# Optimization experiments

Hardware: AMD Instinct MI355X
Metric: run time of the kernel (lower is better)

The kernel has to match this reference:

```python
import jax, jax.numpy as jnp
import numpy as np

B, L_IN, C_IN, C_SKIP, C_OUT, DEPTH = 8, 512, 512, 512, 512, 4
D_INNER, D_STATE, D_CONV, DT_RANK = 1024, 16, 4, 32
EPS = 1e-5


def rmsnorm(x, w):
    return x * jax.lax.rsqrt(jnp.mean(x * x, axis=-1, keepdims=True) + EPS) * w


def layernorm(x, w, b):
    m = jnp.mean(x, axis=-1, keepdims=True)
    v = jnp.mean((x - m) ** 2, axis=-1, keepdims=True)
    return (x - m) * jax.lax.rsqrt(v + EPS) * w + b


def selective_scan(u, dt, A, Bm, Cm, Dp):
    # u, dt: (B, L, Di); A: (Di, N); Bm, Cm: (B, L, N); Dp: (Di,)
    def step(h, inp):
        dt_t, B_t, C_t, u_t = inp  # (B,Di),(B,N),(B,N),(B,Di)
        dA = jnp.exp(dt_t[..., None] * A)            # (B,Di,N)
        h = dA * h + (dt_t * u_t)[..., None] * B_t[:, None, :]
        y = jnp.einsum('bdn,bn->bd', h, C_t)
        return h, y

    Bb, L, Di = u.shape
    h0 = jnp.zeros((Bb, Di, A.shape[1]), u.dtype)
    xs = (dt.transpose(1, 0, 2), Bm.transpose(1, 0, 2),
          Cm.transpose(1, 0, 2), u.transpose(1, 0, 2))
    _, ys = jax.lax.scan(step, h0, xs)               # ys: (L,B,Di)
    return ys.transpose(1, 0, 2) + u * Dp


def mamba_block(x, in_w, cw, cb, xp_w, dtw, dtb, A_log, Dp, ow, ob):
    xz = x @ in_w.T                                   # (B,L,2*Di)
    xc, z = jnp.split(xz, 2, axis=-1)
    # causal depthwise conv, kernel D_CONV
    xc_t = jax.lax.conv_general_dilated(
        xc.transpose(0, 2, 1), cw[:, None, :], (1,), [(D_CONV - 1, 0)],
        feature_group_count=D_INNER,
        dimension_numbers=('NCH', 'OIH', 'NCH'))
    xc = jax.nn.silu((xc_t + cb[None, :, None]).transpose(0, 2, 1))
    xdbc = xc @ xp_w.T                                # (B,L,DT_RANK+2N)
    dtp = xdbc[..., :DT_RANK]
    Bm = xdbc[..., DT_RANK:DT_RANK + D_STATE]
    Cm = xdbc[..., DT_RANK + D_STATE:]
    dt = jax.nn.softplus(dtp @ dtw.T + dtb)
    A = -jnp.exp(A_log)
    y = selective_scan(xc, dt, A, Bm, Cm, Dp)
    return (y * jax.nn.silu(z)) @ ow.T + ob


def forward(motion_input, skip_feats, embed, w_up, b_up, w1, b1, rms_w, w2, b2,
            ln_w, ln_b, in_proj_w, conv_w, conv_b, x_proj_w, dt_proj_w,
            dt_proj_b, A_log, D_param, out_proj_w, out_proj_b,
            norm_f_w, norm_f_b):
    Bb, Lin, C = motion_input.shape
    # ConvTranspose1d(C, C, kernel=2, stride=2): non-overlapping expansion
    up = jnp.einsum('blc,cok->blko', motion_input, w_up)
    up = up.reshape(Bb, Lin * 2, C) + b_up            # (B, 2L, C)
    x = jnp.concatenate([up, skip_feats], axis=-1)    # (B, 2L, C+skip)
    # MLP: Linear -> RMSNorm -> SiLU -> Linear
    x = jax.nn.silu(rmsnorm(x @ w1.T + b1, rms_w)) @ w2.T + b2
    # MotionMamba: add embed, depth residual mamba blocks, final norm
    x = x + embed[:, None, :]
    for i in range(DEPTH):
        x = x + mamba_block(layernorm(x, ln_w[i], ln_b[i]), in_proj_w[i],
                            conv_w[i], conv_b[i], x_proj_w[i], dt_proj_w[i],
                            dt_proj_b[i], A_log[i], D_param[i],
                            out_proj_w[i], out_proj_b[i])
    return layernorm(x, norm_f_w, norm_f_b)


def setup_inputs():
    key = jax.random.key(0)
    ks = jax.random.split(key, 16)
    f = lambda k, sh: jax.random.normal(k, sh, jnp.float32) * 0.02
    inp = {}
    inp['motion_input'] = jax.random.normal(ks[0], (B, L_IN, C_IN), jnp.float32)
    inp['skip_feats'] = jax.random.normal(ks[1], (B, 2 * L_IN, C_SKIP), jnp.float32)
    inp['embed'] = jax.random.normal(ks[2], (B, C_OUT), jnp.float32)
    inp['w_up'] = f(ks[3], (C_IN, C_IN, 2))
    inp['b_up'] = jnp.zeros((C_IN,), jnp.float32)
    inp['w1'] = f(ks[4], (C_OUT, C_IN + C_SKIP))
    inp['b1'] = jnp.zeros((C_OUT,), jnp.float32)
    inp['rms_w'] = jnp.ones((C_OUT,), jnp.float32)
    inp['w2'] = f(ks[5], (C_OUT, C_OUT))
    inp['b2'] = jnp.zeros((C_OUT,), jnp.float32)
    inp['ln_w'] = jnp.ones((DEPTH, C_OUT), jnp.float32)
    inp['ln_b'] = jnp.zeros((DEPTH, C_OUT), jnp.float32)
    inp['in_proj_w'] = f(ks[6], (DEPTH, 2 * D_INNER, C_OUT))
    inp['conv_w'] = f(ks[7], (DEPTH, D_INNER, D_CONV))
    inp['conv_b'] = jnp.zeros((DEPTH, D_INNER), jnp.float32)
    inp['x_proj_w'] = f(ks[8], (DEPTH, DT_RANK + 2 * D_STATE, D_INNER))
    inp['dt_proj_w'] = f(ks[9], (DEPTH, D_INNER, DT_RANK))
    inp['dt_proj_b'] = jnp.full((DEPTH, D_INNER), -4.0, jnp.float32)
    inp['A_log'] = jnp.log(jnp.tile(jnp.arange(1, D_STATE + 1, dtype=jnp.float32), (DEPTH, D_INNER, 1)))
    inp['D_param'] = jnp.ones((DEPTH, D_INNER), jnp.float32)
    inp['out_proj_w'] = f(ks[10], (DEPTH, C_OUT, D_INNER))
    inp['out_proj_b'] = jnp.zeros((DEPTH, C_OUT), jnp.float32)
    inp['norm_f_w'] = jnp.ones((C_OUT,), jnp.float32)
    inp['norm_f_b'] = jnp.zeros((C_OUT,), jnp.float32)
    return inp


def reference(motion_input, skip_feats, embed, w_up, b_up, w1, b1, rms_w, w2,
              b2, ln_w, ln_b, in_proj_w, conv_w, conv_b, x_proj_w, dt_proj_w,
              dt_proj_b, A_log, D_param, out_proj_w, out_proj_b,
              norm_f_w, norm_f_b):
    return forward(motion_input, skip_feats, embed, w_up, b_up, w1, b1, rms_w,
                   w2, b2, ln_w, ln_b, in_proj_w, conv_w, conv_b, x_proj_w,
                   dt_proj_w, dt_proj_b, A_log, D_param, out_proj_w,
                   out_proj_b, norm_f_w, norm_f_b)
```

## Files before the change

kernel.cpp:

```cpp
#include <hip/hip_runtime.h>
#include <cstdint>
#include <cstddef>

#define DEV_INLINE __device__ __forceinline__

static constexpr float EPS = 1e-5f;

DEV_INLINE float sigmoidf_(float x) { return 1.0f / (1.0f + __expf(-x)); }
DEV_INLINE float siluf_(float x) { return x * sigmoidf_(x); }
DEV_INLINE float softplus_fast(float x) {
    return fmaxf(x, 0.0f) + __logf(1.0f + __expf(-fabsf(x)));
}
DEV_INLINE unsigned short f2bf(float x) {
    unsigned u = __builtin_bit_cast(unsigned, x);
    u += 0x7FFFu + ((u >> 16) & 1u);
    return (unsigned short)(u >> 16);
}
DEV_INLINE float bf2f(unsigned short s) {
    unsigned u = ((unsigned)s) << 16;
    return __builtin_bit_cast(float, u);
}

typedef __attribute__((ext_vector_type(8))) short bf16x8;
typedef __attribute__((ext_vector_type(4))) float f32x4;

DEV_INLINE void gload16(const unsigned short* src, char* ldsdst) {
    __builtin_amdgcn_global_load_lds(
        (const __attribute__((address_space(1))) unsigned int*)src,
        (__attribute__((address_space(3))) unsigned int*)ldsdst, 16, 0, 0);
}

DEV_INLINE void cvt8(const float* __restrict__ s, unsigned short* __restrict__ d, int t) {
    float4 f0 = *(const float4*)(s + (size_t)t * 8);
    float4 f1 = *(const float4*)(s + (size_t)t * 8 + 4);
    union { unsigned short u[8]; uint4 v; } pk;
    pk.u[0] = f2bf(f0.x); pk.u[1] = f2bf(f0.y); pk.u[2] = f2bf(f0.z); pk.u[3] = f2bf(f0.w);
    pk.u[4] = f2bf(f1.x); pk.u[5] = f2bf(f1.y); pk.u[6] = f2bf(f1.z); pk.u[7] = f2bf(f1.w);
    *(uint4*)(d + (size_t)t * 8) = pk.v;
}

__global__ __launch_bounds__(256) void prep_all(
    const float* __restrict__ motion, const float* __restrict__ wup,
    const float* __restrict__ w1, const float* __restrict__ w2,
    const float* __restrict__ in_proj_w, const float* __restrict__ out_proj_w,
    const float* __restrict__ x_proj_w, const float* __restrict__ dt_proj_w,
    unsigned short* __restrict__ mbf, unsigned short* __restrict__ wupT,
    unsigned short* __restrict__ w1b, unsigned short* __restrict__ w2b,
    unsigned short* __restrict__ lw)
{
    int bid = (int)blockIdx.x, tid = (int)threadIdx.x;
    if (bid < 1024) {
        cvt8(motion, mbf, bid * 256 + tid);
    } else if (bid < 2048) {
        int t = (bid - 1024) * 256 + tid;
        int c = t >> 9, o = t & 511;
        float2 v = *(const float2*)(wup + (size_t)t * 2);
        wupT[(size_t)o * 512 + c] = f2bf(v.x);
        wupT[262144 + (size_t)o * 512 + c] = f2bf(v.y);
    } else if (bid < 2304) {
        cvt8(w1, w1b, (bid - 2048) * 256 + tid);
    } else if (bid < 2432) {
        cvt8(w2, w2b, (bid - 2304) * 256 + tid);
    } else {
        int r = bid - 2432;
        int layer = r / 816;
        int lb = r - layer * 816;
        unsigned short* base = lw + (size_t)layer * 1671168;
        if (lb < 512) {
            cvt8(in_proj_w + (size_t)layer * 1048576, base, lb * 256 + tid);
        } else if (lb < 768) {
            cvt8(out_proj_w + (size_t)layer * 524288, base + 1048576,
                 (lb - 512) * 256 + tid);
        } else if (lb < 800) {
            cvt8(x_proj_w + (size_t)layer * 65536, base + 1572864,
                 (lb - 768) * 256 + tid);
        } else {
            cvt8(dt_proj_w + (size_t)layer * 32768, base + 1638400,
                 (lb - 800) * 256 + tid);
        }
    }
}

template <int ACT, bool ACC, bool EMBED, bool OBF>
__global__ __launch_bounds__(256) void gemm_mfma(
    const unsigned short* __restrict__ A, int lda,
    const unsigned short* __restrict__ W, int ldw,
    void* __restrict__ Cv, int ldc, int N, int K, int gx,
    const float* __restrict__ bias, const float* __restrict__ embed)
{
    __shared__ unsigned short Asm[2][128 * 64];
    __shared__ unsigned short Wsm[2][128 * 64];
    const int tid = (int)threadIdx.x;
    const int lane = tid & 63;
    const int wv = tid >> 6;
    const int wm = wv >> 1, wn = wv & 1;

    const int nwg = (int)gridDim.x;
    const int lin = (int)blockIdx.x;
    const int logical = (lin & 7) * (nwg >> 3) + (lin >> 3);
    const int by = logical / gx;
    const int bx = logical - by * gx;
    const int bm = by * 128, bn = bx * 128;

    f32x4 acc[4][4] = {};
    const int l8 = lane >> 3;
    const int wc = lane & 7;
    const int wcg = wc ^ l8;
    const int NT = K >> 6;

    {
        char* aB = (char*)Asm[0];
        char* bB = (char*)Wsm[0];
#pragma unroll
        for (int i = 0; i < 4; ++i) {
            int rb = (i * 4 + wv) * 8;
            gload16(W + (size_t)(bn + rb + l8) * ldw + wcg * 8, bB + rb * 128);
            gload16(A + (size_t)(bm + rb + l8) * lda + wcg * 8, aB + rb * 128);
        }
    }
    __syncthreads();

    for (int t = 0; t < NT; ++t) {
        const int cur = t & 1;
        if (t + 1 < NT) {
            const int k1 = (t + 1) << 6;
            char* aB = (char*)Asm[cur ^ 1];
            char* bB = (char*)Wsm[cur ^ 1];
#pragma unroll
            for (int i = 0; i < 4; ++i) {
                int rb = (i * 4 + wv) * 8;
                gload16(W + (size_t)(bn + rb + l8) * ldw + k1 + wcg * 8, bB + rb * 128);
                gload16(A + (size_t)(bm + rb + l8) * lda + k1 + wcg * 8, aB + rb * 128);
            }
        }
        const char* aB = (const char*)Asm[cur];
        const char* bB = (const char*)Wsm[cur];
        const int rA = wm * 64 + (lane & 15);
        const int rB = wn * 64 + (lane & 15);
        const int q = lane >> 4;
#pragma unroll
        for (int kk = 0; kk < 2; ++kk) {
            bf16x8 af[4], bfr[4];
#pragma unroll
            for (int mi = 0; mi < 4; ++mi) {
                int row = rA + mi * 16;
                int ch = (kk * 4 + q) ^ (row & 7);
                af[mi] = *(const bf16x8*)(aB + row * 128 + ch * 16);
            }
#pragma unroll
            for (int ni = 0; ni < 4; ++ni) {
                int row = rB + ni * 16;
                int ch = (kk * 4 + q) ^ (row & 7);
                bfr[ni] = *(const bf16x8*)(bB + row * 128 + ch * 16);
            }
#pragma unroll
            for (int mi = 0; mi < 4; ++mi)
#pragma unroll
                for (int ni = 0; ni < 4; ++ni)
                    acc[mi][ni] = __builtin_amdgcn_mfma_f32_16x16x32_bf16(
                        af[mi], bfr[ni], acc[mi][ni], 0, 0, 0);
        }
        __syncthreads();
    }

    const int cn = lane & 15;
    const int r0 = (lane >> 4) * 4;
    const int eb = EMBED ? (bm >> 10) * N : 0;
#pragma unroll
    for (int ni = 0; ni < 4; ++ni) {
        int col = bn + wn * 64 + ni * 16 + cn;
        float add = bias ? bias[col] : 0.0f;
        if (EMBED) add += embed[eb + col];
#pragma unroll
        for (int mi = 0; mi < 4; ++mi) {
#pragma unroll
            for (int r = 0; r < 4; ++r) {
                int row = bm + wm * 64 + mi * 16 + r0 + r;
                float v = acc[mi][ni][r] + add;
                if (ACT == 1) v = softplus_fast(v);
                if (OBF) {
                    ((unsigned short*)Cv)[(size_t)row * ldc + col] = f2bf(v);
                } else {
                    float* p = (float*)Cv + (size_t)row * ldc + col;
                    if (ACC) *p += v; else *p = v;
                }
            }
        }
    }
}

template <int ACT, bool ACC, bool EMBED, bool OBF, bool UPS>
__global__ __launch_bounds__(256) void gemm_mfma64(
    const unsigned short* __restrict__ A, int lda,
    const unsigned short* __restrict__ W, int ldw,
    void* __restrict__ Cv, int ldc, int N, int K, int gx,
    const float* __restrict__ bias, const float* __restrict__ embed)
{
    __shared__ unsigned short Asm[2][64 * 64];
    __shared__ unsigned short Wsm[2][64 * 64];
    const int tid = (int)threadIdx.x;
    const int lane = tid & 63;
    const int wv = tid >> 6;
    const int wm = wv >> 1, wn = wv & 1;

    const int nwg = (int)gridDim.x;
    const int lin = (int)blockIdx.x;
    const int logical = (lin & 7) * (nwg >> 3) + (lin >> 3);
    const int by = logical / gx;
    const int bx = logical - by * gx;
    const int bm = by * 64, bn = bx * 64;

    f32x4 acc[2][2] = {};
    const int l8 = lane >> 3;
    const int wc = lane & 7;
    const int wcg = wc ^ l8;
    const int NT = K >> 6;

    {
        char* aB = (char*)Asm[0];
        char* bB = (char*)Wsm[0];
#pragma unroll
        for (int i = 0; i < 2; ++i) {
            int rb = (i * 4 + wv) * 8;
            gload16(W + (size_t)(bn + rb + l8) * ldw + wcg * 8, bB + rb * 128);
            gload16(A + (size_t)(bm + rb + l8) * lda + wcg * 8, aB + rb * 128);
        }
    }
    __syncthreads();

    for (int t = 0; t < NT; ++t) {
        const int cur = t & 1;
        if (t + 1 < NT) {
            const int k1 = (t + 1) << 6;
            char* aB = (char*)Asm[cur ^ 1];
            char* bB = (char*)Wsm[cur ^ 1];
#pragma unroll
            for (int i = 0; i < 2; ++i) {
                int rb = (i * 4 + wv) * 8;
                gload16(W + (size_t)(bn + rb + l8) * ldw + k1 + wcg * 8, bB + rb * 128);
                gload16(A + (size_t)(bm + rb + l8) * lda + k1 + wcg * 8, aB + rb * 128);
            }
        }
        const char* aB = (const char*)Asm[cur];
        const char* bB = (const char*)Wsm[cur];
        const int rA = wm * 32 + (lane & 15);
        const int rB = wn * 32 + (lane & 15);
        const int q = lane >> 4;
#pragma unroll
        for (int kk = 0; kk < 2; ++kk) {
            bf16x8 af[2], bfr[2];
#pragma unroll
            for (int mi = 0; mi < 2; ++mi) {
                int row = rA + mi * 16;
                int ch = (kk * 4 + q) ^ (row & 7);
                af[mi] = *(const bf16x8*)(aB + row * 128 + ch * 16);
            }
#pragma unroll
            for (int ni = 0; ni < 2; ++ni) {
                int row = rB + ni * 16;
                int ch = (kk * 4 + q) ^ (row & 7);
                bfr[ni] = *(const bf16x8*)(bB + row * 128 + ch * 16);
            }
#pragma unroll
            for (int mi = 0; mi < 2; ++mi)
#pragma unroll
                for (int ni = 0; ni < 2; ++ni)
                    acc[mi][ni] = __builtin_amdgcn_mfma_f32_16x16x32_bf16(
                        af[mi], bfr[ni], acc[mi][ni], 0, 0, 0);
        }
        __syncthreads();
    }

    const int cn = lane & 15;
    const int r0 = (lane >> 4) * 4;
    const int eb = EMBED ? (bm >> 10) * N : 0;
#pragma unroll
    for (int ni = 0; ni < 2; ++ni) {
        int col = bn + wn * 32 + ni * 16 + cn;
        float add = bias ? bias[UPS ? (col & 511) : col] : 0.0f;
        if (EMBED) add += embed[eb + col];
#pragma unroll
        for (int mi = 0; mi < 2; ++mi) {
#pragma unroll
            for (int r = 0; r < 4; ++r) {
                int row = bm + wm * 32 + mi * 16 + r0 + r;
                float v = acc[mi][ni][r] + add;
                if (ACT == 1) v = softplus_fast(v);
                if (UPS) {
                    size_t ad = (size_t)row * 2048 + ((col >> 9) << 10) + (col & 511);
                    ((unsigned short*)Cv)[ad] = f2bf(v);
                } else if (OBF) {
                    ((unsigned short*)Cv)[(size_t)row * ldc + col] = f2bf(v);
                } else {
                    float* p = (float*)Cv + (size_t)row * ldc + col;
                    if (ACC) *p += v; else *p = v;
                }
            }
        }
    }
}

__global__ __launch_bounds__(256) void gemm_dt(
    const unsigned short* __restrict__ xdbc,
    const unsigned short* __restrict__ wdt,
    const float* __restrict__ bias,
    unsigned short* __restrict__ out)
{
    __shared__ unsigned short S[128 * 136];
    const int tid = (int)threadIdx.x;
    const int lane = tid & 63;
    const int wv = tid >> 6;
    const int wm = wv >> 1, wn = wv & 1;

    const int lin = (int)blockIdx.x;
    const int logical = (lin & 7) * 64 + (lin >> 3);
    const int bm = (logical >> 3) * 128;
    const int bn = (logical & 7) * 128;

    const int fr = lane & 15;
    const int q = lane >> 4;

    bf16x8 af[4], wf[4];
#pragma unroll
    for (int mi = 0; mi < 4; ++mi)
        af[mi] = *(const bf16x8*)(xdbc + (size_t)(bm + wm * 64 + mi * 16 + fr) * 64 + q * 8);
#pragma unroll
    for (int ni = 0; ni < 4; ++ni)
        wf[ni] = *(const bf16x8*)(wdt + (size_t)(bn + wn * 64 + ni * 16 + fr) * 32 + q * 8);

    f32x4 acc[4][4] = {};
#pragma unroll
    for (int mi = 0; mi < 4; ++mi)
#pragma unroll
        for (int ni = 0; ni < 4; ++ni)
            acc[mi][ni] = __builtin_amdgcn_mfma_f32_16x16x32_bf16(
                af[mi], wf[ni], acc[mi][ni], 0, 0, 0);

    const int cn = lane & 15;
    const int r0 = (lane >> 4) * 4;
#pragma unroll
    for (int ni = 0; ni < 4; ++ni) {
        int lcol = wn * 64 + ni * 16 + cn;
        float add = bias[bn + lcol];
#pragma unroll
        for (int mi = 0; mi < 4; ++mi) {
#pragma unroll
            for (int r = 0; r < 4; ++r) {
                int lrow = wm * 64 + mi * 16 + r0 + r;
                S[lrow * 136 + lcol] = f2bf(softplus_fast(acc[mi][ni][r] + add));
            }
        }
    }
    __syncthreads();

    const int row = tid >> 1;
    const int half = tid & 1;
    const unsigned short* src = S + row * 136 + half * 64;
    unsigned short* dst = out + (size_t)(bm + row) * 1024 + bn + half * 64;
#pragma unroll
    for (int k = 0; k < 8; ++k) {
        uint4 v = *(const uint4*)(src + k * 8);
        *(uint4*)(dst + k * 8) = v;
    }
}

__global__ __launch_bounds__(128) void gemm_xdbc(
    const unsigned short* __restrict__ A,
    const unsigned short* __restrict__ W,
    unsigned short* __restrict__ C)
{
    __shared__ unsigned short Asm[64 * 64];
    __shared__ unsigned short Wsm[64 * 64];
    const int tid = (int)threadIdx.x;
    const int lane = tid & 63;
    const int w = tid >> 6;
    const int bm = blockIdx.x * 64;
    const int l8 = lane >> 3, wc = lane & 7, wcg = wc ^ l8;
    char* aB = (char*)Asm;
    char* bB = (char*)Wsm;

    f32x4 acc[2][4] = {};

    for (int k0 = 0; k0 < 1024; k0 += 64) {
#pragma unroll
        for (int i = 0; i < 4; ++i) {
            int rb = (i * 2 + w) * 8;
            gload16(A + (size_t)(bm + rb + l8) * 1024 + k0 + wcg * 8, aB + rb * 128);
            gload16(W + (size_t)(rb + l8) * 1024 + k0 + wcg * 8, bB + rb * 128);
        }
        __syncthreads();
        const int rA = w * 32 + (lane & 15);
        const int rB = (lane & 15);
        const int q = lane >> 4;
#pragma unroll
        for (int kk = 0; kk < 2; ++kk) {
            bf16x8 af[2], bfr[4];
#pragma unroll
            for (int mi = 0; mi < 2; ++mi) {
                int row = rA + mi * 16;
                int ch = (kk * 4 + q) ^ (row & 7);
                af[mi] = *(const bf16x8*)(aB + row * 128 + ch * 16);
            }
#pragma unroll
            for (int ni = 0; ni < 4; ++ni) {
                int row = rB + ni * 16;
                int ch = (kk * 4 + q) ^ (row & 7);
                bfr[ni] = *(const bf16x8*)(bB + row * 128 + ch * 16);
            }
#pragma unroll
            for (int mi = 0; mi < 2; ++mi)
#pragma unroll
                for (int ni = 0; ni < 4; ++ni)
                    acc[mi][ni] = __builtin_amdgcn_mfma_f32_16x16x32_bf16(
                        af[mi], bfr[ni], acc[mi][ni], 0, 0, 0);
        }
        __syncthreads();
    }
    const int cn = lane & 15;
    const int r0 = (lane >> 4) * 4;
#pragma unroll
    for (int mi = 0; mi < 2; ++mi)
#pragma unroll
        for (int ni = 0; ni < 4; ++ni)
#pragma unroll
            for (int r = 0; r < 4; ++r) {
                int row = bm + w * 32 + mi * 16 + r0 + r;
                C[(size_t)row * 64 + ni * 16 + cn] = f2bf(acc[mi][ni][r]);
            }
}

__global__ __launch_bounds__(256) void concat_skip(
    const float* __restrict__ skip, unsigned short* __restrict__ x0)
{
    int t = blockIdx.x * 256 + (int)threadIdx.x;
    int row = t >> 6;
    int c8 = (t & 63) << 3;
    const float* s = skip + (size_t)row * 512 + c8;
    float4 f0 = *(const float4*)s;
    float4 f1 = *(const float4*)(s + 4);
    union { unsigned short u[8]; uint4 v; } pk;
    pk.u[0] = f2bf(f0.x); pk.u[1] = f2bf(f0.y); pk.u[2] = f2bf(f0.z); pk.u[3] = f2bf(f0.w);
    pk.u[4] = f2bf(f1.x); pk.u[5] = f2bf(f1.y); pk.u[6] = f2bf(f1.z); pk.u[7] = f2bf(f1.w);
    *(uint4*)(x0 + (size_t)row * 1024 + 512 + c8) = pk.v;
}

template <bool BFOUT>
__global__ __launch_bounds__(256) void layernorm_k(
    const float* __restrict__ x, void* __restrict__ outp,
    const float* __restrict__ w, const float* __restrict__ b)
{
    const int row = blockIdx.x * 4 + ((int)threadIdx.x >> 6);
    const int lane = (int)threadIdx.x & 63;
    const float* xr = x + (size_t)row * 512;
    float4 v0 = *(const float4*)(xr + lane * 4);
    float4 v1 = *(const float4*)(xr + 256 + lane * 4);
    float s = v0.x + v0.y + v0.z + v0.w + v1.x + v1.y + v1.z + v1.w;
    float q = v0.x*v0.x + v0.y*v0.y + v0.z*v0.z + v0.w*v0.w
            + v1.x*v1.x + v1.y*v1.y + v1.z*v1.z + v1.w*v1.w;
#pragma unroll
    for (int o = 32; o; o >>= 1) {
        s += __shfl_xor(s, o, 64);
        q += __shfl_xor(q, o, 64);
    }
    const float mean = s * (1.0f / 512.0f);
    const float var = q * (1.0f / 512.0f) - mean * mean;
    const float rstd = rsqrtf(var + EPS);
    float4 w0 = *(const float4*)(w + lane * 4);
    float4 w1 = *(const float4*)(w + 256 + lane * 4);
    float4 b0 = *(const float4*)(b + lane * 4);
    float4 b1 = *(const float4*)(b + 256 + lane * 4);
    float4 o0, o1;
    o0.x = (v0.x - mean) * rstd * w0.x + b0.x;
    o0.y = (v0.y - mean) * rstd * w0.y + b0.y;
    o0.z = (v0.z - mean) * rstd * w0.z + b0.z;
    o0.w = (v0.w - mean) * rstd * w0.w + b0.w;
    o1.x = (v1.x - mean) * rstd * w1.x + b1.x;
    o1.y = (v1.y - mean) * rstd * w1.y + b1.y;
    o1.z = (v1.z - mean) * rstd * w1.z + b1.z;
    o1.w = (v1.w - mean) * rstd * w1.w + b1.w;
    if (BFOUT) {
        unsigned short* ob = (unsigned short*)outp + (size_t)row * 512;
        union { unsigned short u[4]; uint2 v; } p0, p1;
        p0.u[0] = f2bf(o0.x); p0.u[1] = f2bf(o0.y); p0.u[2] = f2bf(o0.z); p0.u[3] = f2bf(o0.w);
        p1.u[0] = f2bf(o1.x); p1.u[1] = f2bf(o1.y); p1.u[2] = f2bf(o1.z); p1.u[3] = f2bf(o1.w);
        *(uint2*)(ob + lane * 4) = p0.v;
        *(uint2*)(ob + 256 + lane * 4) = p1.v;
    } else {
        float* orow = (float*)outp + (size_t)row * 512;
        *(float4*)(orow + lane * 4) = o0;
        *(float4*)(orow + 256 + lane * 4) = o1;
    }
}

__global__ __launch_bounds__(256) void rms_silu_k(
    const float* __restrict__ x, unsigned short* __restrict__ o,
    const float* __restrict__ w)
{
    const int row = blockIdx.x * 4 + ((int)threadIdx.x >> 6);
    const int lane = (int)threadIdx.x & 63;
    const float* xr = x + (size_t)row * 512;
    float4 v0 = *(const float4*)(xr + lane * 4);
    float4 v1 = *(const float4*)(xr + 256 + lane * 4);
    float q = v0.x*v0.x + v0.y*v0.y + v0.z*v0.z + v0.w*v0.w
            + v1.x*v1.x + v1.y*v1.y + v1.z*v1.z + v1.w*v1.w;
#pragma unroll
    for (int of = 32; of; of >>= 1) q += __shfl_xor(q, of, 64);
    const float scale = rsqrtf(q * (1.0f / 512.0f) + EPS);
    float4 w0 = *(const float4*)(w + lane * 4);
    float4 w1 = *(const float4*)(w + 256 + lane * 4);
    union { unsigned short u[4]; uint2 v; } p0, p1;
    p0.u[0] = f2bf(siluf_(v0.x * scale * w0.x));
    p0.u[1] = f2bf(siluf_(v0.y * scale * w0.y));
    p0.u[2] = f2bf(siluf_(v0.z * scale * w0.z));
    p0.u[3] = f2bf(siluf_(v0.w * scale * w0.w));
    p1.u[0] = f2bf(siluf_(v1.x * scale * w1.x));
    p1.u[1] = f2bf(siluf_(v1.y * scale * w1.y));
    p1.u[2] = f2bf(siluf_(v1.z * scale * w1.z));
    p1.u[3] = f2bf(siluf_(v1.w * scale * w1.w));
    unsigned short* ob = o + (size_t)row * 512;
    *(uint2*)(ob + lane * 4) = p0.v;
    *(uint2*)(ob + 256 + lane * 4) = p1.v;
}

__global__ __launch_bounds__(256) void conv_silu_k2(
    const unsigned short* __restrict__ xz, unsigned short* __restrict__ ub,
    const float* __restrict__ cw, const float* __restrict__ cb)
{
    int t = blockIdx.x * 256 + (int)threadIdx.x;
    int d = t & 1023;
    int bc = t >> 10;
    int b = bc >> 4, ch = bc & 15;
    int l0 = ch * 64;
    float4 w4 = *(const float4*)(cw + (size_t)d * 4);
    float bias = cb[d];
    const unsigned short* src = xz + ((size_t)(b * 1024 + l0)) * 2048 + d;
    unsigned short* dst = ub + ((size_t)(b * 1024 + l0)) * 1024 + d;
    float x0 = 0.f, x1 = 0.f, x2 = 0.f;
    if (l0 > 0) {
        x0 = bf2f(src[-(size_t)3 * 2048]);
        x1 = bf2f(src[-(size_t)2 * 2048]);
        x2 = bf2f(src[-(size_t)1 * 2048]);
    }
    for (int l = 0; l < 64; ++l) {
        float x3 = bf2f(src[(size_t)l * 2048]);
        float v = fmaf(x0, w4.x, fmaf(x1, w4.y, fmaf(x2, w4.z, fmaf(x3, w4.w, bias))));
        dst[(size_t)l * 1024] = f2bf(siluf_(v));
        x0 = x1; x1 = x2; x2 = x3;
    }
}

template <int CTRL>
DEV_INLINE float dpp_f(float x) {
    int yi = __builtin_amdgcn_update_dpp(
        0, __builtin_bit_cast(int, x), CTRL, 0xF, 0xF, true);
    return __builtin_bit_cast(float, yi);
}

template <int PHASE>
__global__ __launch_bounds__(256) void scan5(
    const unsigned short* __restrict__ dtp,
    const unsigned short* ubf,
    unsigned short* ybf,
    const unsigned short* __restrict__ xdbc,
    const unsigned short* __restrict__ zbf,
    float* __restrict__ hp,
    const float* __restrict__ A_log,
    const float* __restrict__ Dp)
{
    __shared__ float SDT2[16][260];
    __shared__ float SB[32][20];
    __shared__ float SC[PHASE == 2 ? 32 : 1][20];
    __shared__ float YS[PHASE == 2 ? 32 : 1][68];

    const int lin = (int)blockIdx.x;
    const int logical = (lin & 7) * 256 + (lin >> 3);
    const int gg = logical & 15;
    const int t2 = logical >> 4;
    const int ch = t2 & 15, b = t2 >> 4;
    if (PHASE == 1 && ch == 15) return;
    const int tid = (int)threadIdx.x;
    const int dl = tid >> 2, q = tid & 2 ? (tid & 3) : (tid & 3);
    const int qq = tid & 3;
    const int dblk = gg << 6;
    const int d = dblk + dl;
    const int m0 = b * 1024 + ch * 64;

    float An[4];
#pragma unroll
    for (int j = 0; j < 4; ++j)
        An[j] = -__expf(A_log[(size_t)d * 16 + qq * 4 + j]);

    float h[4] = {};
    float prod[4] = {1.f, 1.f, 1.f, 1.f};
    if (PHASE == 2) {
        const float* hpb = hp + (((size_t)(b * 1024 + d)) * 16) * 32 + qq * 8;
        for (int cc = 0; cc < ch; ++cc) {
            float4 v0 = *(const float4*)(hpb + cc * 32);
            float4 v1 = *(const float4*)(hpb + cc * 32 + 4);
            h[0] = fmaf(v0.y, h[0], v0.x);
            h[1] = fmaf(v0.w, h[1], v0.z);
            h[2] = fmaf(v1.y, h[2], v1.x);
            h[3] = fmaf(v1.w, h[3], v1.z);
        }
    }

    const int sl2 = tid >> 4;
    const int sdg = (tid & 15) * 4;
    const int bcr = (tid & 127) >> 2;
    const int bne = (tid & 3) << 2;

    for (int s = 0; s < 2; ++s) {
        const int lbase = s * 32;
        {
            size_t r0 = (size_t)(m0 + lbase + 2 * sl2);
            uint2 dA = *(const uint2*)(dtp + r0 * 1024 + dblk + sdg);
            uint2 dB = *(const uint2*)(dtp + (r0 + 1) * 1024 + dblk + sdg);
            uint2 uA = *(const uint2*)(ubf + r0 * 1024 + dblk + sdg);
            uint2 uB = *(const uint2*)(ubf + (r0 + 1) * 1024 + dblk + sdg);
            const unsigned short* da = (const unsigned short*)&dA;
            const unsigned short* db = (const unsigned short*)&dB;
            const unsigned short* ua = (const unsigned short*)&uA;
            const unsigned short* ub2 = (const unsigned short*)&uB;
#pragma unroll
            for (int j = 0; j < 4; ++j) {
                float d0 = bf2f(da[j]), d1 = bf2f(db[j]);
                float4 wv = {d0, d0 * bf2f(ua[j]), d1, d1 * bf2f(ub2[j])};
                *(float4*)&SDT2[sl2][(sdg + j) * 4] = wv;
            }
        }
        {
            size_t gr = (size_t)(m0 + lbase + bcr);
            if (tid < 128) {
                uint2 Bu = *(const uint2*)(xdbc + gr * 64 + 32 + bne);
                const unsigned short* bb = (const unsigned short*)&Bu;
                float4 bv = {bf2f(bb[0]), bf2f(bb[1]), bf2f(bb[2]), bf2f(bb[3])};
                *(float4*)&SB[bcr][bne] = bv;
            } else if (PHASE == 2) {
                uint2 Cu = *(const uint2*)(xdbc + gr * 64 + 48 + bne);
                const unsigned short* cc2 = (const unsigned short*)&Cu;
                float4 cv = {bf2f(cc2[0]), bf2f(cc2[1]), bf2f(cc2[2]), bf2f(cc2[3])};
                *(float4*)&SC[bcr][bne] = cv;
            }
        }
        __syncthreads();

        for (int l2 = 0; l2 < 16; ++l2) {
            float4 sd = *(const float4*)&SDT2[l2][dl * 4];
            float4 B0 = *(const float4*)&SB[2 * l2][qq * 4];
            float4 B1 = *(const float4*)&SB[2 * l2 + 1][qq * 4];
            float p0 = 0.0f, p1 = 0.0f;
            float4 C0, C1;
            if (PHASE == 2) {
                C0 = *(const float4*)&SC[2 * l2][qq * 4];
                C1 = *(const float4*)&SC[2 * l2 + 1][qq * 4];
            }
            const float* B0p = (const float*)&B0;
            const float* B1p = (const float*)&B1;
            const float* C0p = (const float*)&C0;
            const float* C1p = (const float*)&C1;
#pragma unroll
            for (int j = 0; j < 4; ++j) {
                float e0 = __expf(sd.x * An[j]);
                if (PHASE == 1) prod[j] *= e0;
                h[j] = fmaf(e0, h[j], sd.y * B0p[j]);
                if (PHASE == 2) p0 = fmaf(h[j], C0p[j], p0);
                float e1 = __expf(sd.z * An[j]);
                if (PHASE == 1) prod[j] *= e1;
                h[j] = fmaf(e1, h[j], sd.w * B1p[j]);
                if (PHASE == 2) p1 = fmaf(h[j], C1p[j], p1);
            }
            if (PHASE == 2) {
                p0 += dpp_f<0xB1>(p0);
                p0 += dpp_f<0x4E>(p0);
                p1 += dpp_f<0xB1>(p1);
                p1 += dpp_f<0x4E>(p1);
                if (qq == 0) {
                    YS[2 * l2][dl] = p0;
                    YS[2 * l2 + 1][dl] = p1;
                }
            }
        }
        __syncthreads();

        if (PHASE == 2) {
            const int row = tid >> 3;
            const int e8 = (tid & 7) * 8;
            size_t gr = (size_t)(m0 + lbase + row);
            float4 p40 = *(const float4*)&YS[row][e8];
            float4 p41 = *(const float4*)&YS[row][e8 + 4];
            uint4 uu = *(const uint4*)(ubf + gr * 1024 + dblk + e8);
            uint4 zz = *(const uint4*)(zbf + gr * 2048 + 1024 + dblk + e8);
            float4 D0 = *(const float4*)(Dp + dblk + e8);
            float4 D1 = *(const float4*)(Dp + dblk + e8 + 4);
            const unsigned short* up = (const unsigned short*)&uu;
            const unsigned short* zp = (const unsigned short*)&zz;
            const float* pp0 = (const float*)&p40;
            const float* pp1 = (const float*)&p41;
            const float* dd0 = (const float*)&D0;
            const float* dd1 = (const float*)&D1;
            union { unsigned short u[8]; uint4 v; } pk;
#pragma unroll
            for (int j = 0; j < 4; ++j) {
                float y = fmaf(bf2f(up[j]), dd0[j], pp0[j]) * siluf_(bf2f(zp[j]));
                pk.u[j] = f2bf(y);
            }
#pragma unroll
            for (int j = 0; j < 4; ++j) {
                float y = fmaf(bf2f(up[4 + j]), dd1[j], pp1[j]) * siluf_(bf2f(zp[4 + j]));
                pk.u[4 + j] = f2bf(y);
            }
            *(uint4*)(ybf + gr * 1024 + dblk + e8) = pk.v;
        }
        __syncthreads();
    }

    if (PHASE == 1) {
        float* hpo = hp + (((size_t)(b * 1024 + d) * 16 + ch)) * 32 + qq * 8;
        float4 o0 = {h[0], prod[0], h[1], prod[1]};
        float4 o1 = {h[2], prod[2], h[3], prod[3]};
        *(float4*)hpo = o0;
        *(float4*)(hpo + 4) = o1;
    }
}

extern "C" void kernel_launch(void* const* d_in, const int* in_sizes, int n_in,
                              void* d_out, int out_size, void* d_ws, size_t ws_size,
                              hipStream_t stream)
{
    const float* motion     = (const float*)d_in[0];
    const float* skip       = (const float*)d_in[1];
    const float* embed      = (const float*)d_in[2];
    const float* w_up       = (const float*)d_in[3];
    const float* b_up       = (const float*)d_in[4];
    const float* w1         = (const float*)d_in[5];
    const float* b1         = (const float*)d_in[6];
    const float* rms_w      = (const float*)d_in[7];
    const float* w2         = (const float*)d_in[8];
    const float* b2         = (const float*)d_in[9];
    const float* ln_w       = (const float*)d_in[10];
    const float* ln_b       = (const float*)d_in[11];
    const float* in_proj_w  = (const float*)d_in[12];
    const float* conv_w     = (const float*)d_in[13];
    const float* conv_b     = (const float*)d_in[14];
    const float* x_proj_w   = (const float*)d_in[15];
    const float* dt_proj_w  = (const float*)d_in[16];
    const float* dt_proj_b  = (const float*)d_in[17];
    const float* A_log      = (const float*)d_in[18];
    const float* D_param    = (const float*)d_in[19];
    const float* out_proj_w = (const float*)d_in[20];
    const float* out_proj_b = (const float*)d_in[21];
    const float* norm_f_w   = (const float*)d_in[22];
    const float* norm_f_b   = (const float*)d_in[23];
    float* out = (float*)d_out;
    float* ws = (float*)d_ws;

    float* xbuf = ws;
    float* xlnf = ws + 4194304;
    unsigned short* xzbf  = (unsigned short*)(ws + 8388608);
    unsigned short* ubf   = (unsigned short*)(ws + 16777216);
    unsigned short* dtybf = (unsigned short*)(ws + 20971520);
    unsigned short* xdbc  = (unsigned short*)(ws + 25165824);
    float* hp  = ws + 25427968;
    unsigned short* xsbf = (unsigned short*)(ws + 29622272);
    unsigned short* mbf  = (unsigned short*)(ws + 31719424);
    unsigned short* wupT = (unsigned short*)(ws + 32768000);
    unsigned short* w1b  = (unsigned short*)(ws + 33030144);
    unsigned short* w2b  = (unsigned short*)(ws + 33292288);
    unsigned short* lw   = (unsigned short*)(ws + 33423360);

    unsigned short* x0bf = xzbf;

    dim3 blk(256);

    prep_all<<<dim3(5696), blk, 0, stream>>>(
        motion, w_up, w1, w2, in_proj_w, out_proj_w, x_proj_w, dt_proj_w,
        mbf, wupT, w1b, w2b, lw);

    gemm_mfma64<0, false, false, true, true><<<dim3(1024), blk, 0, stream>>>(
        mbf, 512, wupT, 512, x0bf, 0, 1024, 512, 16, b_up, nullptr);
    concat_skip<<<dim3(2048), blk, 0, stream>>>(skip, x0bf);

    gemm_mfma64<0, false, false, false, false><<<dim3(1024), blk, 0, stream>>>(
        x0bf, 1024, w1b, 1024, xlnf, 512, 512, 1024, 8, b1, nullptr);
    rms_silu_k<<<dim3(2048), blk, 0, stream>>>(xlnf, xsbf, rms_w);

    gemm_mfma64<0, false, true, false, false><<<dim3(1024), blk, 0, stream>>>(
        xsbf, 512, w2b, 512, xbuf, 512, 512, 512, 8, b2, embed);

    for (int i = 0; i < 4; ++i) {
        unsigned short* ipw = lw + (size_t)i * 1671168;
        unsigned short* opw = ipw + 1048576;
        unsigned short* xpw = ipw + 1572864;
        unsigned short* wdt = ipw + 1638400;
        layernorm_k<true><<<dim3(2048), blk, 0, stream>>>(
            xbuf, xsbf, ln_w + (size_t)i * 512, ln_b + (size_t)i * 512);
        gemm_mfma<0, false, false, true><<<dim3(1024), blk, 0, stream>>>(
            xsbf, 512, ipw, 512, xzbf, 2048, 2048, 512, 16, nullptr, nullptr);
        conv_silu_k2<<<dim3(512), blk, 0, stream>>>(
            xzbf, ubf, conv_w + (size_t)i * 4096, conv_b + (size_t)i * 1024);
        gemm_xdbc<<<dim3(128), dim3(128), 0, stream>>>(ubf, xpw, xdbc);
        gemm_dt<<<dim3(512), blk, 0, stream>>>(
            xdbc, wdt, dt_proj_b + (size_t)i * 1024, dtybf);
        scan5<1><<<dim3(2048), blk, 0, stream>>>(
            dtybf, ubf, nullptr, xdbc, xzbf, hp,
            A_log + (size_t)i * 16384, D_param + (size_t)i * 1024);
        scan5<2><<<dim3(2048), blk, 0, stream>>>(
            dtybf, ubf, ubf, xdbc, xzbf, hp,
            A_log + (size_t)i * 16384, D_param + (size_t)i * 1024);
        gemm_mfma64<0, true, false, false, false><<<dim3(1024), blk, 0, stream>>>(
            ubf, 1024, opw, 1024, xbuf, 512, 512, 1024, 8,
            out_proj_b + (size_t)i * 512, nullptr);
    }

    layernorm_k<false><<<dim3(2048), blk, 0, stream>>>(xbuf, out, norm_f_w, norm_f_b);
}
```

Measured before the change: 692.3 us.

## Lengthen scan chunks to 128 steps and prefetch next tile into registers

```diff
diff --git a/kernel.cpp b/kernel.cpp
--- a/kernel.cpp
+++ b/kernel.cpp
@@ -557,7 +557,7 @@
 }
 
 template <int PHASE>
-__global__ __launch_bounds__(256) void scan5(
+__global__ __launch_bounds__(256) void scan6(
     const unsigned short* __restrict__ dtp,
     const unsigned short* ubf,
     unsigned short* ybf,
@@ -567,23 +567,24 @@
     const float* __restrict__ A_log,
     const float* __restrict__ Dp)
 {
-    __shared__ float SDT2[16][260];
+    __shared__ float SDT[64 * 68];
     __shared__ float SB[32][20];
     __shared__ float SC[PHASE == 2 ? 32 : 1][20];
     __shared__ float YS[PHASE == 2 ? 32 : 1][68];
 
     const int lin = (int)blockIdx.x;
-    const int logical = (lin & 7) * 256 + (lin >> 3);
+    const int logical = (lin & 7) * 128 + (lin >> 3);
     const int gg = logical & 15;
-    const int t2 = logical >> 4;
-    const int ch = t2 & 15, b = t2 >> 4;
-    if (PHASE == 1 && ch == 15) return;
+    const int r = logical >> 4;
+    const int c = r & 7, b = r >> 3;
+    if (PHASE == 1 && c == 7) return;
     const int tid = (int)threadIdx.x;
-    const int dl = tid >> 2, q = tid & 2 ? (tid & 3) : (tid & 3);
-    const int qq = tid & 3;
+    const int dl = tid >> 2, qq = tid & 3;
+    const int wv = tid >> 6;
+    const int lane = tid & 63;
     const int dblk = gg << 6;
     const int d = dblk + dl;
-    const int m0 = b * 1024 + ch * 64;
+    const int m0 = b * 1024 + c * 128;
 
     float An[4];
 #pragma unroll
@@ -593,8 +594,8 @@
     float h[4] = {};
     float prod[4] = {1.f, 1.f, 1.f, 1.f};
     if (PHASE == 2) {
-        const float* hpb = hp + (((size_t)(b * 1024 + d)) * 16) * 32 + qq * 8;
-        for (int cc = 0; cc < ch; ++cc) {
+        const float* hpb = hp + ((size_t)(b * 1024 + d)) * 256 + qq * 8;
+        for (int cc = 0; cc < c; ++cc) {
             float4 v0 = *(const float4*)(hpb + cc * 32);
             float4 v1 = *(const float4*)(hpb + cc * 32 + 4);
             h[0] = fmaf(v0.y, h[0], v0.x);
@@ -604,48 +605,64 @@
         }
     }
 
-    const int sl2 = tid >> 4;
-    const int sdg = (tid & 15) * 4;
     const int bcr = (tid & 127) >> 2;
     const int bne = (tid & 3) << 2;
 
-    for (int s = 0; s < 2; ++s) {
+    unsigned short rdt0[4], rdt1[4], ru0[4], ru1[4];
+    uint2 rBC;
+
+#pragma unroll
+    for (int j = 0; j < 4; ++j) {
+        size_t r0 = (size_t)(m0 + 2 * (wv * 4 + j));
+        rdt0[j] = dtp[r0 * 1024 + dblk + lane];
+        rdt1[j] = dtp[(r0 + 1) * 1024 + dblk + lane];
+        ru0[j]  = ubf[r0 * 1024 + dblk + lane];
+        ru1[j]  = ubf[(r0 + 1) * 1024 + dblk + lane];
+    }
+    if (tid < 128) {
+        rBC = *(const uint2*)(xdbc + (size_t)(m0 + bcr) * 64 + 32 + bne);
+    } else if (PHASE == 2) {
+        rBC = *(const uint2*)(xdbc + (size_t)(m0 + bcr) * 64 + 48 + bne);
+    }
+
+    for (int s = 0; s < 4; ++s) {
         const int lbase = s * 32;
-        {
-            size_t r0 = (size_t)(m0 + lbase + 2 * sl2);
-            uint2 dA = *(const uint2*)(dtp + r0 * 1024 + dblk + sdg);
-            uint2 dB = *(const uint2*)(dtp + (r0 + 1) * 1024 + dblk + sdg);
-            uint2 uA = *(const uint2*)(ubf + r0 * 1024 + dblk + sdg);
-            uint2 uB = *(const uint2*)(ubf + (r0 + 1) * 1024 + dblk + sdg);
-            const unsigned short* da = (const unsigned short*)&dA;
-            const unsigned short* db = (const unsigned short*)&dB;
-            const unsigned short* ua = (const unsigned short*)&uA;
-            const unsigned short* ub2 = (const unsigned short*)&uB;
+        if (PHASE == 1 && s > 0) __syncthreads();
+#pragma unroll
+        for (int j = 0; j < 4; ++j) {
+            float d0 = bf2f(rdt0[j]), d1 = bf2f(rdt1[j]);
+            float4 wvv = {d0, d0 * bf2f(ru0[j]), d1, d1 * bf2f(ru1[j])};
+            *(float4*)&SDT[lane * 68 + (wv * 4 + j) * 4] = wvv;
+        }
+        if (tid < 128) {
+            const unsigned short* bb = (const unsigned short*)&rBC;
+            float4 bv = {bf2f(bb[0]), bf2f(bb[1]), bf2f(bb[2]), bf2f(bb[3])};
+            *(float4*)&SB[bcr][bne] = bv;
+        } else if (PHASE == 2) {
+            const unsigned short* cc2 = (const unsigned short*)&rBC;
+            float4 cv = {bf2f(cc2[0]), bf2f(cc2[1]), bf2f(cc2[2]), bf2f(cc2[3])};
+            *(float4*)&SC[bcr][bne] = cv;
+        }
+        if (s < 3) {
+            const int nb = lbase + 32;
 #pragma unroll
             for (int j = 0; j < 4; ++j) {
-                float d0 = bf2f(da[j]), d1 = bf2f(db[j]);
-                float4 wv = {d0, d0 * bf2f(ua[j]), d1, d1 * bf2f(ub2[j])};
-                *(float4*)&SDT2[sl2][(sdg + j) * 4] = wv;
-            }
-        }
-        {
-            size_t gr = (size_t)(m0 + lbase + bcr);
+                size_t r0 = (size_t)(m0 + nb + 2 * (wv * 4 + j));
+                rdt0[j] = dtp[r0 * 1024 + dblk + lane];
+                rdt1[j] = dtp[(r0 + 1) * 1024 + dblk + lane];
+                ru0[j]  = ubf[r0 * 1024 + dblk + lane];
+                ru1[j]  = ubf[(r0 + 1) * 1024 + dblk + lane];
+            }
             if (tid < 128) {
-                uint2 Bu = *(const uint2*)(xdbc + gr * 64 + 32 + bne);
-                const unsigned short* bb = (const unsigned short*)&Bu;
-                float4 bv = {bf2f(bb[0]), bf2f(bb[1]), bf2f(bb[2]), bf2f(bb[3])};
-                *(float4*)&SB[bcr][bne] = bv;
+                rBC = *(const uint2*)(xdbc + (size_t)(m0 + nb + bcr) * 64 + 32 + bne);
             } else if (PHASE == 2) {
-                uint2 Cu = *(const uint2*)(xdbc + gr * 64 + 48 + bne);
-                const unsigned short* cc2 = (const unsigned short*)&Cu;
-                float4 cv = {bf2f(cc2[0]), bf2f(cc2[1]), bf2f(cc2[2]), bf2f(cc2[3])};
-                *(float4*)&SC[bcr][bne] = cv;
+                rBC = *(const uint2*)(xdbc + (size_t)(m0 + nb + bcr) * 64 + 48 + bne);
             }
         }
         __syncthreads();
 
         for (int l2 = 0; l2 < 16; ++l2) {
-            float4 sd = *(const float4*)&SDT2[l2][dl * 4];
+            float4 sd = *(const float4*)&SDT[dl * 68 + l2 * 4];
             float4 B0 = *(const float4*)&SB[2 * l2][qq * 4];
             float4 B1 = *(const float4*)&SB[2 * l2 + 1][qq * 4];
             float p0 = 0.0f, p1 = 0.0f;
@@ -680,9 +697,9 @@
                 }
             }
         }
-        __syncthreads();
 
         if (PHASE == 2) {
+            __syncthreads();
             const int row = tid >> 3;
             const int e8 = (tid & 7) * 8;
             size_t gr = (size_t)(m0 + lbase + row);
@@ -709,13 +726,13 @@
                 float y = fmaf(bf2f(up[4 + j]), dd1[j], pp1[j]) * siluf_(bf2f(zp[4 + j]));
                 pk.u[4 + j] = f2bf(y);
             }
+            __syncthreads();
             *(uint4*)(ybf + gr * 1024 + dblk + e8) = pk.v;
         }
-        __syncthreads();
     }
 
     if (PHASE == 1) {
-        float* hpo = hp + (((size_t)(b * 1024 + d) * 16 + ch)) * 32 + qq * 8;
+        float* hpo = hp + ((size_t)(b * 1024 + d)) * 256 + c * 32 + qq * 8;
         float4 o0 = {h[0], prod[0], h[1], prod[1]};
         float4 o1 = {h[2], prod[2], h[3], prod[3]};
         *(float4*)hpo = o0;
@@ -801,10 +818,10 @@
         gemm_xdbc<<<dim3(128), dim3(128), 0, stream>>>(ubf, xpw, xdbc);
         gemm_dt<<<dim3(512), blk, 0, stream>>>(
             xdbc, wdt, dt_proj_b + (size_t)i * 1024, dtybf);
-        scan5<1><<<dim3(2048), blk, 0, stream>>>(
+        scan6<1><<<dim3(1024), blk, 0, stream>>>(
             dtybf, ubf, nullptr, xdbc, xzbf, hp,
             A_log + (size_t)i * 16384, D_param + (size_t)i * 1024);
-        scan5<2><<<dim3(2048), blk, 0, stream>>>(
+        scan6<2><<<dim3(1024), blk, 0, stream>>>(
             dtybf, ubf, ubf, xdbc, xzbf, hp,
             A_log + (size_t)i * 16384, D_param + (size_t)i * 1024);
         gemm_mfma64<0, true, false, false, false><<<dim3(1024), blk, 0, stream>>>(
```

Result: no change. 698.6 us (+0.9%).
